# Performance work log

Hardware: AMD Instinct MI355X
Metric: run time of the kernel (lower is better)

## Reference

```python
import jax, jax.numpy as jnp
import numpy as np

NUM_EXPERTS = 32
TOP_K = 4
ALPHA = 1.702   # GPT-OSS GLU alpha
LIMIT = 7.0     # GPT-OSS clamp limit


def setup_inputs() -> dict:
    key = jax.random.key(0)
    ks = jax.random.split(key, 7)
    B, S, H, E = 2, 2048, 1024, NUM_EXPERTS
    return {
        "hidden_states": jax.random.normal(ks[0], (B, S, H), jnp.float32),
        "router_weight": jax.random.normal(ks[1], (E, H), jnp.float32) * 0.02,
        "router_bias": jax.random.normal(ks[2], (E,), jnp.float32) * 0.02,
        "gate_up_proj": jax.random.normal(ks[3], (E, H, 2 * H), jnp.float32) * 0.02,
        "gate_up_proj_bias": jax.random.normal(ks[4], (E, 2 * H), jnp.float32) * 0.02,
        "down_proj": jax.random.normal(ks[5], (E, H, H), jnp.float32) * 0.02,
        "down_proj_bias": jax.random.normal(ks[6], (E, H), jnp.float32) * 0.02,
    }


def _moe_forward(hidden_states, router_weight, router_bias,
                 gate_up_proj, gate_up_proj_bias, down_proj, down_proj_bias):
    B, S, H = hidden_states.shape
    E, K = NUM_EXPERTS, TOP_K
    T = B * S
    capacity = T * K // E * 2  # expert_capacity as in the torch module

    x = hidden_states.reshape(T, H)

    # ---- router: linear -> top-k -> softmax over top-k -> dense scatter ----
    logits = x @ router_weight.T + router_bias                     # [T, E]
    top_vals, top_idx = jax.lax.top_k(logits, K)                   # [T, K]
    weights = jax.nn.softmax(top_vals, axis=-1)                    # [T, K]
    router_scores = jnp.zeros_like(logits).at[
        jnp.arange(T)[:, None], top_idx].set(weights)              # [T, E]

    # ---- capacity-based dispatch (first-come-first-served in token order) ----
    flat_e = top_idx.reshape(-1)                                   # [T*K]
    token_id = jnp.repeat(jnp.arange(T), K)                        # [T*K]
    onehot = (flat_e[:, None] == jnp.arange(E)[None, :]).astype(jnp.int32)
    # rank of each assignment within its expert (0-based, arrival order)
    rank = jnp.take_along_axis(jnp.cumsum(onehot, axis=0),
                               flat_e[:, None], axis=1)[:, 0] - 1  # [T*K]
    valid = rank < capacity
    slot = jnp.where(valid, rank, capacity)  # out-of-range slot -> dropped

    buffer = jnp.zeros((E, capacity, H), x.dtype).at[flat_e, slot].set(
        x[token_id], mode="drop")                                  # [E, C, H]

    # ---- grouped expert MLP: gate_up GEMM + GPT-OSS GLU + down GEMM ----
    gu = jnp.einsum("ech,ehf->ecf", buffer, gate_up_proj) \
         + gate_up_proj_bias[:, None, :]                           # [E, C, 2H]
    gate = gu[..., ::2]
    up = gu[..., 1::2]
    gate = jnp.minimum(gate, LIMIT)
    up = jnp.clip(up, -LIMIT, LIMIT)
    glu = gate * jax.nn.sigmoid(gate * ALPHA)
    act = (up + 1.0) * glu                                         # [E, C, H]
    expert_out = jnp.einsum("ech,ehf->ecf", act, down_proj) \
                 + down_proj_bias[:, None, :]                      # [E, C, H]

    # ---- weighted combine (dropped tokens contribute zero) ----
    gathered = expert_out[flat_e, jnp.where(valid, rank, 0)]       # [T*K, H]
    w = router_scores[token_id, flat_e] * valid.astype(x.dtype)    # [T*K]
    out = jax.ops.segment_sum(gathered * w[:, None], token_id,
                              num_segments=T)                      # [T, H]
    return out.reshape(B, S, H), router_scores


def reference(hidden_states, router_weight, router_bias, gate_up_proj,
              gate_up_proj_bias, down_proj, down_proj_bias):
    return _moe_forward(hidden_states, router_weight, router_bias,
                        gate_up_proj, gate_up_proj_bias, down_proj,
                        down_proj_bias)
```

## Files before the change

kernel.cpp:

```cpp
#include <hip/hip_runtime.h>
#include <hip/hip_bf16.h>

#define T_TOK 4096
#define H_DIM 1024
#define E_EXP 32
#define TOPK 4
#define CAP 1024
#define PAIRS (T_TOK*TOPK)

typedef __attribute__((ext_vector_type(8))) short short8v;
typedef __attribute__((ext_vector_type(4))) float f32x4;
typedef unsigned long long u64;
typedef unsigned short ushort;

__device__ __forceinline__ float bf16_bits_to_f32(ushort h) {
    return __uint_as_float(((unsigned)h) << 16);
}
__device__ __forceinline__ unsigned bf16r(float f) {
    unsigned u = __float_as_uint(f);
    return ((u + 0x7fffu + ((u >> 16) & 1u)) >> 16) & 0xffffu;
}
__device__ __forceinline__ unsigned cvt2(float a, float b) {
    unsigned r;
    asm("v_cvt_pk_bf16_f32 %0, %1, %2" : "=v"(r) : "v"(a), "v"(b));
    return r;
}

#define GLD16(gsrc, ldst) \
    __builtin_amdgcn_global_load_lds( \
        (const __attribute__((address_space(1))) unsigned*)(gsrc), \
        (__attribute__((address_space(3))) unsigned*)(ldst), 16, 0, 0)

__global__ __launch_bounds__(256) void router_kernel(
    const float* __restrict__ x, const float* __restrict__ rw,
    const float* __restrict__ rb, float* __restrict__ scores,
    int* __restrict__ flat_e, float* __restrict__ flat_w)
{
    __shared__ float xs[H_DIM];
    __shared__ float lg[E_EXP];
    __shared__ float sw[TOPK];
    __shared__ int   se[TOPK];
    const int t = blockIdx.x;
    const int tid = threadIdx.x;

    for (int i = tid; i < H_DIM; i += 256) xs[i] = x[(size_t)t * H_DIM + i];
    __syncthreads();

    const int e = tid >> 3, l8 = tid & 7;
    float partial = 0.f;
    const float* wr = rw + (size_t)e * H_DIM;
    for (int h = l8; h < H_DIM; h += 8) partial += xs[h] * wr[h];
    partial += __shfl_xor(partial, 1);
    partial += __shfl_xor(partial, 2);
    partial += __shfl_xor(partial, 4);
    if (l8 == 0) lg[e] = partial + rb[e];
    __syncthreads();

    if (tid == 0) {
        unsigned used = 0;
        float bv[TOPK]; int bi[TOPK];
        #pragma unroll
        for (int j = 0; j < TOPK; j++) {
            float best = -1e30f; int bid = -1;
            for (int q = 0; q < E_EXP; q++) {
                if (used & (1u << q)) continue;
                if (lg[q] > best) { best = lg[q]; bid = q; }
            }
            used |= 1u << bid;
            bv[j] = best; bi[j] = bid;
        }
        const float m = bv[0];
        float s = 0.f; float w[TOPK];
        #pragma unroll
        for (int j = 0; j < TOPK; j++) { w[j] = expf(bv[j] - m); s += w[j]; }
        const float inv = 1.f / s;
        #pragma unroll
        for (int j = 0; j < TOPK; j++) { sw[j] = w[j] * inv; se[j] = bi[j]; }
    }
    __syncthreads();

    if (tid < E_EXP) {
        float v = 0.f;
        #pragma unroll
        for (int j = 0; j < TOPK; j++) if (se[j] == tid) v = sw[j];
        scores[(size_t)t * E_EXP + tid] = v;
    }
    if (tid < TOPK) {
        flat_e[t * TOPK + tid] = se[tid];
        flat_w[t * TOPK + tid] = sw[tid];
    }
}

__global__ __launch_bounds__(256) void scan_kernel(
    const int* __restrict__ flat_e, const float* __restrict__ flat_w,
    int* __restrict__ slot_token, float* __restrict__ slot_w,
    int* __restrict__ pair_slot, int* __restrict__ counts)
{
    __shared__ int cnt[256 * E_EXP];
    const int tid = threadIdx.x;
    for (int e = 0; e < E_EXP; e++) cnt[tid * E_EXP + e] = 0;
    __syncthreads();
    const int base = tid * (PAIRS / 256);
    for (int i = 0; i < PAIRS / 256; i++) {
        int e = flat_e[base + i];
        cnt[tid * E_EXP + e]++;
    }
    __syncthreads();
    if (tid < E_EXP) {
        int run = 0;
        for (int i = 0; i < 256; i++) {
            int idx = i * E_EXP + tid;
            int v = cnt[idx];
            cnt[idx] = run;
            run += v;
        }
        counts[tid] = min(run, CAP);
    }
    __syncthreads();
    for (int i = 0; i < PAIRS / 256; i++) {
        int p = base + i;
        int e = flat_e[p];
        int r = cnt[tid * E_EXP + e]++;
        if (r < CAP) {
            slot_token[e * CAP + r] = p >> 2;
            slot_w[e * CAP + r] = flat_w[p];
            pair_slot[p] = r;
        } else {
            pair_slot[p] = -1;
        }
    }
}

__global__ __launch_bounds__(256) void stage_tokens(
    const float* __restrict__ x, const int* __restrict__ slot_token,
    const int* __restrict__ counts, char* __restrict__ xbuf)
{
    const int e = blockIdx.y, rt = blockIdx.x;
    const int n = counts[e];
    const int row0 = rt * 128;
    if (row0 >= n) return;
    const int rows_here = min(128, n - row0);
    const int lane = threadIdx.x & 63, wv = threadIdx.x >> 6;
    char* tb = xbuf + ((size_t)(e * 8 + rt)) * 262144;

    for (int r = wv; r < rows_here; r += 4) {
        const float* xr = x + (size_t)slot_token[e * CAP + row0 + r] * H_DIM;
        const int s = (r >> 1) & 3;
        #pragma unroll
        for (int half = 0; half < 2; ++half) {
            int gi = half * 64 + lane;
            float4 a = *(const float4*)(xr + gi * 8);
            float4 b = *(const float4*)(xr + gi * 8 + 4);
            uint4 w;
            w.x = cvt2(a.x, a.y); w.y = cvt2(a.z, a.w);
            w.z = cvt2(b.x, b.y); w.w = cvt2(b.z, b.w);
            int t = gi >> 2, kq = gi & 3;
            *(uint4*)(tb + (size_t)t * 8192 + r * 64 + ((kq ^ s) * 16)) = w;
        }
    }
}

__global__ __launch_bounds__(256) void conv_gu(
    const float* __restrict__ wgu, char* __restrict__ wbuf)
{
    const int ct = blockIdx.x;
    const int tseg = blockIdx.y;
    const int e = blockIdx.z;
    const int lane = threadIdx.x & 63, wv = threadIdx.x >> 6;
    char* dst_base = wbuf + ((size_t)(e * 16 + ct) * 32) * 8192;
    #pragma unroll
    for (int i = 0; i < 2; ++i) {
        const int t = tseg * 8 + wv * 2 + i;
        const float* src = wgu + ((size_t)e * 1024 + t * 32) * 2048 + ct * 128 + 2 * lane;
        float2 v[32];
        #pragma unroll
        for (int k = 0; k < 32; ++k) v[k] = *(const float2*)(src + (size_t)k * 2048);
        char* dst = dst_base + (size_t)t * 8192 + lane * 16;
        #pragma unroll
        for (int kq = 0; kq < 4; ++kq) {
            uint4 g, u;
            g.x = cvt2(v[kq*8+0].x, v[kq*8+1].x); g.y = cvt2(v[kq*8+2].x, v[kq*8+3].x);
            g.z = cvt2(v[kq*8+4].x, v[kq*8+5].x); g.w = cvt2(v[kq*8+6].x, v[kq*8+7].x);
            u.x = cvt2(v[kq*8+0].y, v[kq*8+1].y); u.y = cvt2(v[kq*8+2].y, v[kq*8+3].y);
            u.z = cvt2(v[kq*8+4].y, v[kq*8+5].y); u.w = cvt2(v[kq*8+6].y, v[kq*8+7].y);
            *(uint4*)(dst + kq * 1024) = g;
            *(uint4*)(dst + 4096 + kq * 1024) = u;
        }
    }
}

__global__ __launch_bounds__(256) void conv_dn(
    const float* __restrict__ wd, char* __restrict__ wbuf)
{
    const int ct = blockIdx.x;
    const int tseg = blockIdx.y;
    const int e = blockIdx.z;
    const int lane = threadIdx.x & 63, wv = threadIdx.x >> 6;
    const int t = tseg * 4 + wv;
    const float* src = wd + ((size_t)e * 1024 + t * 32) * 1024 + ct * 128 + 2 * lane;
    float2 v[32];
    #pragma unroll
    for (int k = 0; k < 32; ++k) v[k] = *(const float2*)(src + (size_t)k * 1024);
    char* dst = wbuf + (((size_t)(e * 8 + ct) * 32) + t) * 8192 + (2 * lane) * 16;
    #pragma unroll
    for (int kq = 0; kq < 4; ++kq) {
        uint4 g0, g1;
        g0.x = cvt2(v[kq*8+0].x, v[kq*8+1].x); g0.y = cvt2(v[kq*8+2].x, v[kq*8+3].x);
        g0.z = cvt2(v[kq*8+4].x, v[kq*8+5].x); g0.w = cvt2(v[kq*8+6].x, v[kq*8+7].x);
        g1.x = cvt2(v[kq*8+0].y, v[kq*8+1].y); g1.y = cvt2(v[kq*8+2].y, v[kq*8+3].y);
        g1.z = cvt2(v[kq*8+4].y, v[kq*8+5].y); g1.w = cvt2(v[kq*8+6].y, v[kq*8+7].y);
        *(uint4*)(dst + kq * 2048) = g0;
        *(uint4*)(dst + kq * 2048 + 16) = g1;
    }
}

__global__ __launch_bounds__(256, 4) void gateup_mfma(
    const char* __restrict__ xbuf, const char* __restrict__ wbuf,
    const float* __restrict__ gub, const int* __restrict__ counts,
    char* __restrict__ act)
{
    const int lin = blockIdx.x;
    const int xcd = lin & 7, slot = lin >> 3;
    const int gg = (slot >> 3) * 8 + xcd;
    const int rt = slot & 7;
    const int e = gg >> 4, ct = gg & 15;

    const int n = counts[e];
    const int row0 = rt * 128;
    if (row0 >= n) return;
    const int rows_here = min(128, n - row0);
    const int c0f = ct * 64;

    __shared__ char AsB[2][8192];
    __shared__ char BsB[2][8192];

    const int tid = threadIdx.x;
    const int lane = tid & 63, wid = tid >> 6;
    const int wr = wid >> 1, wc = wid & 1;
    const int l15 = lane & 15, l4 = lane >> 4;

    const char* xtile = xbuf + ((size_t)(e * 8 + rt)) * 262144;
    const char* btile = wbuf + ((size_t)(e * 16 + ct) * 32) * 8192;

    f32x4 accg[4][2], accu[4][2];
    #pragma unroll
    for (int m = 0; m < 4; m++)
        #pragma unroll
        for (int j = 0; j < 2; j++) { accg[m][j] = (f32x4)0.f; accu[m][j] = (f32x4)0.f; }

    auto stage = [&](int buf, int t) {
        const char* sa = xtile + (size_t)t * 8192 + tid * 16;
        GLD16(sa, AsB[buf] + tid * 16);
        GLD16(sa + 4096, AsB[buf] + 4096 + tid * 16);
        const char* sb = btile + (size_t)t * 8192 + tid * 16;
        GLD16(sb, BsB[buf] + tid * 16);
        GLD16(sb + 4096, BsB[buf] + 4096 + tid * 16);
    };

    stage(0, 0);
    __syncthreads();
    int cur = 0;
    for (int t = 0; t < 32; ++t) {
        if (t < 31) stage(cur ^ 1, t + 1);

        short8v afr[4];
        #pragma unroll
        for (int m = 0; m < 4; ++m) {
            int row = wr * 64 + m * 16 + l15;
            afr[m] = *(short8v*)(AsB[cur] + row * 64 + ((l4 ^ ((row >> 1) & 3)) * 16));
        }
        __builtin_amdgcn_s_setprio(1);
        #pragma unroll
        for (int j = 0; j < 2; ++j) {
            int fl = wc * 32 + j * 16 + l15;
            short8v bg8 = *(short8v*)(BsB[cur] + l4 * 1024 + fl * 16);
            short8v bu8 = *(short8v*)(BsB[cur] + 4096 + l4 * 1024 + fl * 16);
            #pragma unroll
            for (int m = 0; m < 4; ++m) {
                accg[m][j] = __builtin_amdgcn_mfma_f32_16x16x32_bf16(afr[m], bg8, accg[m][j], 0, 0, 0);
                accu[m][j] = __builtin_amdgcn_mfma_f32_16x16x32_bf16(afr[m], bu8, accu[m][j], 0, 0, 0);
            }
        }
        __builtin_amdgcn_s_setprio(0);
        __syncthreads();
        cur ^= 1;
    }

    char* atile = act + ((size_t)(e * 8 + rt)) * 262144;
    #pragma unroll
    for (int j = 0; j < 2; ++j) {
        int f = c0f + wc * 32 + j * 16 + l15;
        float bgb = gub[(size_t)e * 2048 + 2 * f];
        float bub = gub[(size_t)e * 2048 + 2 * f + 1];
        int tt = f >> 5, kq = (f & 31) >> 3, ke = f & 7;
        #pragma unroll
        for (int m = 0; m < 4; ++m) {
            int rbase = wr * 64 + m * 16 + l4 * 4;
            #pragma unroll
            for (int reg = 0; reg < 4; ++reg) {
                int r = rbase + reg;
                if (r >= rows_here) continue;
                float g = accg[m][j][reg] + bgb;
                float u = accu[m][j][reg] + bub;
                g = fminf(g, 7.0f);
                u = fminf(fmaxf(u, -7.0f), 7.0f);
                float glu = g / (1.0f + __expf(-1.702f * g));
                float a = (u + 1.0f) * glu;
                *(ushort*)(atile + (size_t)tt * 8192 + r * 64 +
                           ((kq ^ ((r >> 1) & 3)) * 16) + ke * 2) = (ushort)bf16r(a);
            }
        }
    }
}

__global__ __launch_bounds__(256, 4) void down_mfma(
    const char* __restrict__ act, const char* __restrict__ wbuf,
    const float* __restrict__ db, const int* __restrict__ counts,
    ushort* __restrict__ eout)
{
    const int lin = blockIdx.x;
    const int xcd = lin & 7, slot = lin >> 3;
    const int gg = (slot >> 3) * 8 + xcd;
    const int rt = slot & 7;
    const int e = gg >> 3, ct = gg & 7;

    const int n = counts[e];
    const int row0 = rt * 128;
    if (row0 >= n) return;
    const int rows_here = min(128, n - row0);
    const int c0 = ct * 128;

    __shared__ char AsB[2][8192];
    __shared__ char BsB[2][8192];

    const int tid = threadIdx.x;
    const int lane = tid & 63, wid = tid >> 6;
    const int wr = wid >> 1, wc = wid & 1;
    const int l15 = lane & 15, l4 = lane >> 4;

    const char* atile = act + ((size_t)(e * 8 + rt)) * 262144;
    const char* btile = wbuf + ((size_t)(e * 8 + ct) * 32) * 8192;

    f32x4 acc[4][4];
    #pragma unroll
    for (int m = 0; m < 4; m++)
        #pragma unroll
        for (int j = 0; j < 4; j++) acc[m][j] = (f32x4)0.f;

    auto stage = [&](int buf, int t) {
        const char* sa = atile + (size_t)t * 8192 + tid * 16;
        GLD16(sa, AsB[buf] + tid * 16);
        GLD16(sa + 4096, AsB[buf] + 4096 + tid * 16);
        const char* sb = btile + (size_t)t * 8192 + tid * 16;
        GLD16(sb, BsB[buf] + tid * 16);
        GLD16(sb + 4096, BsB[buf] + 4096 + tid * 16);
    };

    stage(0, 0);
    __syncthreads();
    int cur = 0;
    for (int t = 0; t < 32; ++t) {
        if (t < 31) stage(cur ^ 1, t + 1);

        short8v afr[4];
        #pragma unroll
        for (int m = 0; m < 4; ++m) {
            int row = wr * 64 + m * 16 + l15;
            afr[m] = *(short8v*)(AsB[cur] + row * 64 + ((l4 ^ ((row >> 1) & 3)) * 16));
        }
        __builtin_amdgcn_s_setprio(1);
        #pragma unroll
        for (int j = 0; j < 4; ++j) {
            int nn = wc * 64 + j * 16 + l15;
            short8v b8 = *(short8v*)(BsB[cur] + l4 * 2048 + nn * 16);
            #pragma unroll
            for (int m = 0; m < 4; ++m)
                acc[m][j] = __builtin_amdgcn_mfma_f32_16x16x32_bf16(afr[m], b8, acc[m][j], 0, 0, 0);
        }
        __builtin_amdgcn_s_setprio(0);
        __syncthreads();
        cur ^= 1;
    }

    #pragma unroll
    for (int j = 0; j < 4; ++j) {
        int col = c0 + wc * 64 + j * 16 + l15;
        float bias = db[(size_t)e * H_DIM + col];
        #pragma unroll
        for (int m = 0; m < 4; ++m) {
            int rbase = wr * 64 + m * 16 + l4 * 4;
            #pragma unroll
            for (int reg = 0; reg < 4; ++reg) {
                int r = rbase + reg;
                if (r >= rows_here) continue;
                eout[((size_t)e * CAP + row0 + r) * H_DIM + col] =
                    (ushort)bf16r(acc[m][j][reg] + bias);
            }
        }
    }
}

__global__ __launch_bounds__(256) void finalize_kernel(
    const ushort* __restrict__ eout, const int* __restrict__ flat_e,
    const float* __restrict__ flat_w, const int* __restrict__ pair_slot,
    float* __restrict__ out)
{
    const int t = blockIdx.x;
    const int c = threadIdx.x * 4;
    float a0 = 0.f, a1 = 0.f, a2 = 0.f, a3 = 0.f;
    #pragma unroll
    for (int k = 0; k < TOPK; ++k) {
        int p = t * TOPK + k;
        int s = pair_slot[p];
        if (s < 0) continue;
        int e = flat_e[p];
        float w = flat_w[p];
        const ushort* row = eout + ((size_t)e * CAP + s) * H_DIM + c;
        ushort4 v = *(const ushort4*)row;
        a0 += w * bf16_bits_to_f32(v.x);
        a1 += w * bf16_bits_to_f32(v.y);
        a2 += w * bf16_bits_to_f32(v.z);
        a3 += w * bf16_bits_to_f32(v.w);
    }
    *(float4*)(out + (size_t)t * H_DIM + c) = make_float4(a0, a1, a2, a3);
}

extern "C" void kernel_launch(void* const* d_in, const int* in_sizes, int n_in,
                              void* d_out, int out_size, void* d_ws, size_t ws_size,
                              hipStream_t stream) {
    const float* x   = (const float*)d_in[0];
    const float* rw  = (const float*)d_in[1];
    const float* rb  = (const float*)d_in[2];
    const float* wgu = (const float*)d_in[3];
    const float* gub = (const float*)d_in[4];
    const float* wd  = (const float*)d_in[5];
    const float* db  = (const float*)d_in[6];

    float* out    = (float*)d_out;
    float* scores = out + (size_t)T_TOK * H_DIM;

    char* ws = (char*)d_ws;
    char* xbuf = ws;
    ushort* eout = (ushort*)ws;
    size_t off = (size_t)E_EXP * CAP * H_DIM * 2;
    char* act     = ws + off;  off += (size_t)E_EXP * CAP * H_DIM * 2;
    char* wbuf_gu = ws + off;  off += (size_t)E_EXP * 16 * 32 * 8192;
    char* wbuf_dn = ws + off;  off += (size_t)E_EXP * 8 * 32 * 8192;
    int*   flat_e     = (int*)(ws + off);   off += PAIRS * 4;
    float* flat_w     = (float*)(ws + off); off += PAIRS * 4;
    int*   slot_token = (int*)(ws + off);   off += E_EXP * CAP * 4;
    float* slot_w     = (float*)(ws + off); off += E_EXP * CAP * 4;
    int*   pair_slot  = (int*)(ws + off);   off += PAIRS * 4;
    int*   counts     = (int*)(ws + off);   off += E_EXP * 4;
    (void)ws_size; (void)out_size; (void)n_in; (void)in_sizes; (void)slot_w;

    hipLaunchKernelGGL(router_kernel, dim3(T_TOK), dim3(256), 0, stream,
                       x, rw, rb, scores, flat_e, flat_w);
    hipLaunchKernelGGL(scan_kernel, dim3(1), dim3(256), 0, stream,
                       flat_e, flat_w, slot_token, slot_w, pair_slot, counts);
    hipLaunchKernelGGL(stage_tokens, dim3(8, E_EXP), dim3(256), 0, stream,
                       x, slot_token, counts, xbuf);
    hipLaunchKernelGGL(conv_gu, dim3(16, 4, E_EXP), dim3(256), 0, stream, wgu, wbuf_gu);
    hipLaunchKernelGGL(conv_dn, dim3(8, 8, E_EXP), dim3(256), 0, stream, wd, wbuf_dn);
    hipLaunchKernelGGL(gateup_mfma, dim3(4096), dim3(256), 0, stream,
                       xbuf, wbuf_gu, gub, counts, act);
    hipLaunchKernelGGL(down_mfma, dim3(2048), dim3(256), 0, stream,
                       act, wbuf_dn, db, counts, eout);
    hipLaunchKernelGGL(finalize_kernel, dim3(T_TOK), dim3(256), 0, stream,
                       eout, flat_e, flat_w, pair_slot, out);
}
```

Baseline: 507.4 us.

## Triple-buffer LDS staging with partial vmcnt waits in MoE GEMMs

```diff
diff --git a/kernel.cpp b/kernel.cpp
--- a/kernel.cpp
+++ b/kernel.cpp
@@ -30,6 +30,11 @@
     __builtin_amdgcn_global_load_lds( \
         (const __attribute__((address_space(1))) unsigned*)(gsrc), \
         (__attribute__((address_space(3))) unsigned*)(ldst), 16, 0, 0)
+
+#define WAIT_VM4() asm volatile("s_waitcnt vmcnt(4)" ::: "memory")
+#define WAIT_VM0() asm volatile("s_waitcnt vmcnt(0)" ::: "memory")
+#define SCHEDB()   __builtin_amdgcn_sched_barrier(0)
+#define BARRIER()  __builtin_amdgcn_s_barrier()
 
 __global__ __launch_bounds__(256) void router_kernel(
     const float* __restrict__ x, const float* __restrict__ rw,
@@ -214,7 +219,7 @@
     }
 }
 
-__global__ __launch_bounds__(256, 4) void gateup_mfma(
+__global__ __launch_bounds__(256, 3) void gateup_mfma(
     const char* __restrict__ xbuf, const char* __restrict__ wbuf,
     const float* __restrict__ gub, const int* __restrict__ counts,
     char* __restrict__ act)
@@ -231,8 +236,8 @@
     const int rows_here = min(128, n - row0);
     const int c0f = ct * 64;
 
-    __shared__ char AsB[2][8192];
-    __shared__ char BsB[2][8192];
+    __shared__ char AsB[3][8192];
+    __shared__ char BsB[3][8192];
 
     const int tid = threadIdx.x;
     const int lane = tid & 63, wid = tid >> 6;
@@ -258,10 +263,13 @@
     };
 
     stage(0, 0);
-    __syncthreads();
-    int cur = 0;
+    stage(1, 1);
+    WAIT_VM4(); SCHEDB();
+    BARRIER(); SCHEDB();
+
+    int cur = 0, dst = 2;
     for (int t = 0; t < 32; ++t) {
-        if (t < 31) stage(cur ^ 1, t + 1);
+        if (t + 2 < 32) stage(dst, t + 2);
 
         short8v afr[4];
         #pragma unroll
@@ -282,8 +290,13 @@
             }
         }
         __builtin_amdgcn_s_setprio(0);
-        __syncthreads();
-        cur ^= 1;
+
+        if (t + 2 < 32) { WAIT_VM4(); }
+        else if (t + 1 < 32) { WAIT_VM0(); }
+        SCHEDB();
+        if (t + 1 < 32) { BARRIER(); SCHEDB(); }
+        cur = (cur == 2) ? 0 : cur + 1;
+        dst = (dst == 2) ? 0 : dst + 1;
     }
 
     char* atile = act + ((size_t)(e * 8 + rt)) * 262144;
@@ -313,7 +326,7 @@
     }
 }
 
-__global__ __launch_bounds__(256, 4) void down_mfma(
+__global__ __launch_bounds__(256, 3) void down_mfma(
     const char* __restrict__ act, const char* __restrict__ wbuf,
     const float* __restrict__ db, const int* __restrict__ counts,
     ushort* __restrict__ eout)
@@ -330,8 +343,8 @@
     const int rows_here = min(128, n - row0);
     const int c0 = ct * 128;
 
-    __shared__ char AsB[2][8192];
-    __shared__ char BsB[2][8192];
+    __shared__ char AsB[3][8192];
+    __shared__ char BsB[3][8192];
 
     const int tid = threadIdx.x;
     const int lane = tid & 63, wid = tid >> 6;
@@ -357,10 +370,13 @@
     };
 
     stage(0, 0);
-    __syncthreads();
-    int cur = 0;
+    stage(1, 1);
+    WAIT_VM4(); SCHEDB();
+    BARRIER(); SCHEDB();
+
+    int cur = 0, dst = 2;
     for (int t = 0; t < 32; ++t) {
-        if (t < 31) stage(cur ^ 1, t + 1);
+        if (t + 2 < 32) stage(dst, t + 2);
 
         short8v afr[4];
         #pragma unroll
@@ -378,8 +394,13 @@
                 acc[m][j] = __builtin_amdgcn_mfma_f32_16x16x32_bf16(afr[m], b8, acc[m][j], 0, 0, 0);
         }
         __builtin_amdgcn_s_setprio(0);
-        __syncthreads();
-        cur ^= 1;
+
+        if (t + 2 < 32) { WAIT_VM4(); }
+        else if (t + 1 < 32) { WAIT_VM0(); }
+        SCHEDB();
+        if (t + 1 < 32) { BARRIER(); SCHEDB(); }
+        cur = (cur == 2) ? 0 : cur + 1;
+        dst = (dst == 2) ? 0 : dst + 1;
     }
 
     #pragma unroll
```

New measurement: 530.3 us. 1.05x slower.

## Fuse gate-up weight conversion into GEMM with LDS-resident weights; batch router tokens

Applied to the files above, without the earlier changes.

```diff
diff --git a/kernel.cpp b/kernel.cpp
--- a/kernel.cpp
+++ b/kernel.cpp
@@ -31,32 +31,50 @@
         (const __attribute__((address_space(1))) unsigned*)(gsrc), \
         (__attribute__((address_space(3))) unsigned*)(ldst), 16, 0, 0)
 
+#define WAIT_VM1() asm volatile("s_waitcnt vmcnt(1)" ::: "memory")
+#define WAIT_VM0() asm volatile("s_waitcnt vmcnt(0)" ::: "memory")
+#define SCHEDB()   __builtin_amdgcn_sched_barrier(0)
+#define BARRIER()  __builtin_amdgcn_s_barrier()
+
 __global__ __launch_bounds__(256) void router_kernel(
     const float* __restrict__ x, const float* __restrict__ rw,
     const float* __restrict__ rb, float* __restrict__ scores,
     int* __restrict__ flat_e, float* __restrict__ flat_w)
 {
-    __shared__ float xs[H_DIM];
-    __shared__ float lg[E_EXP];
-    __shared__ float sw[TOPK];
-    __shared__ int   se[TOPK];
-    const int t = blockIdx.x;
+    __shared__ float xs[8][H_DIM];
+    __shared__ float lg[8][E_EXP];
+    const int t0 = blockIdx.x * 8;
     const int tid = threadIdx.x;
 
-    for (int i = tid; i < H_DIM; i += 256) xs[i] = x[(size_t)t * H_DIM + i];
+    for (int i = tid; i < 2048; i += 256) {
+        int row = i >> 8, c4 = i & 255;
+        *(float4*)&xs[row][c4 * 4] =
+            *(const float4*)(x + (size_t)(t0 + row) * H_DIM + c4 * 4);
+    }
     __syncthreads();
 
     const int e = tid >> 3, l8 = tid & 7;
-    float partial = 0.f;
-    const float* wr = rw + (size_t)e * H_DIM;
-    for (int h = l8; h < H_DIM; h += 8) partial += xs[h] * wr[h];
-    partial += __shfl_xor(partial, 1);
-    partial += __shfl_xor(partial, 2);
-    partial += __shfl_xor(partial, 4);
-    if (l8 == 0) lg[e] = partial + rb[e];
-    __syncthreads();
-
-    if (tid == 0) {
+    float part[8];
+    #pragma unroll
+    for (int tt = 0; tt < 8; ++tt) part[tt] = 0.f;
+    const float* wrow = rw + (size_t)e * H_DIM;
+    for (int h = l8; h < H_DIM; h += 8) {
+        float w = wrow[h];
+        #pragma unroll
+        for (int tt = 0; tt < 8; ++tt) part[tt] = fmaf(xs[tt][h], w, part[tt]);
+    }
+    #pragma unroll
+    for (int tt = 0; tt < 8; ++tt) {
+        float v = part[tt];
+        v += __shfl_xor(v, 1);
+        v += __shfl_xor(v, 2);
+        v += __shfl_xor(v, 4);
+        if (l8 == 0) lg[tt][e] = v + rb[e];
+    }
+    __syncthreads();
+
+    if (tid < 8) {
+        const int tt = tid, t = t0 + tt;
         unsigned used = 0;
         float bv[TOPK]; int bi[TOPK];
         #pragma unroll
@@ -64,7 +82,7 @@
             float best = -1e30f; int bid = -1;
             for (int q = 0; q < E_EXP; q++) {
                 if (used & (1u << q)) continue;
-                if (lg[q] > best) { best = lg[q]; bid = q; }
+                if (lg[tt][q] > best) { best = lg[tt][q]; bid = q; }
             }
             used |= 1u << bid;
             bv[j] = best; bi[j] = bid;
@@ -75,19 +93,18 @@
         for (int j = 0; j < TOPK; j++) { w[j] = expf(bv[j] - m); s += w[j]; }
         const float inv = 1.f / s;
         #pragma unroll
-        for (int j = 0; j < TOPK; j++) { sw[j] = w[j] * inv; se[j] = bi[j]; }
-    }
-    __syncthreads();
-
-    if (tid < E_EXP) {
-        float v = 0.f;
-        #pragma unroll
-        for (int j = 0; j < TOPK; j++) if (se[j] == tid) v = sw[j];
-        scores[(size_t)t * E_EXP + tid] = v;
-    }
-    if (tid < TOPK) {
-        flat_e[t * TOPK + tid] = se[tid];
-        flat_w[t * TOPK + tid] = sw[tid];
+        for (int j = 0; j < TOPK; j++) w[j] *= inv;
+        for (int q = 0; q < E_EXP; ++q) {
+            float v = 0.f;
+            #pragma unroll
+            for (int j = 0; j < TOPK; j++) if (bi[j] == q) v = w[j];
+            scores[(size_t)t * E_EXP + q] = v;
+        }
+        #pragma unroll
+        for (int j = 0; j < TOPK; j++) {
+            flat_e[t * TOPK + j] = bi[j];
+            flat_w[t * TOPK + j] = w[j];
+        }
     }
 }
 
@@ -160,35 +177,6 @@
     }
 }
 
-__global__ __launch_bounds__(256) void conv_gu(
-    const float* __restrict__ wgu, char* __restrict__ wbuf)
-{
-    const int ct = blockIdx.x;
-    const int tseg = blockIdx.y;
-    const int e = blockIdx.z;
-    const int lane = threadIdx.x & 63, wv = threadIdx.x >> 6;
-    char* dst_base = wbuf + ((size_t)(e * 16 + ct) * 32) * 8192;
-    #pragma unroll
-    for (int i = 0; i < 2; ++i) {
-        const int t = tseg * 8 + wv * 2 + i;
-        const float* src = wgu + ((size_t)e * 1024 + t * 32) * 2048 + ct * 128 + 2 * lane;
-        float2 v[32];
-        #pragma unroll
-        for (int k = 0; k < 32; ++k) v[k] = *(const float2*)(src + (size_t)k * 2048);
-        char* dst = dst_base + (size_t)t * 8192 + lane * 16;
-        #pragma unroll
-        for (int kq = 0; kq < 4; ++kq) {
-            uint4 g, u;
-            g.x = cvt2(v[kq*8+0].x, v[kq*8+1].x); g.y = cvt2(v[kq*8+2].x, v[kq*8+3].x);
-            g.z = cvt2(v[kq*8+4].x, v[kq*8+5].x); g.w = cvt2(v[kq*8+6].x, v[kq*8+7].x);
-            u.x = cvt2(v[kq*8+0].y, v[kq*8+1].y); u.y = cvt2(v[kq*8+2].y, v[kq*8+3].y);
-            u.z = cvt2(v[kq*8+4].y, v[kq*8+5].y); u.w = cvt2(v[kq*8+6].y, v[kq*8+7].y);
-            *(uint4*)(dst + kq * 1024) = g;
-            *(uint4*)(dst + 4096 + kq * 1024) = u;
-        }
-    }
-}
-
 __global__ __launch_bounds__(256) void conv_dn(
     const float* __restrict__ wd, char* __restrict__ wbuf)
 {
@@ -214,100 +202,116 @@
     }
 }
 
-__global__ __launch_bounds__(256, 4) void gateup_mfma(
-    const char* __restrict__ xbuf, const char* __restrict__ wbuf,
+__global__ __launch_bounds__(512, 1) void gateup_mfma(
+    const char* __restrict__ xbuf, const float* __restrict__ wgu,
     const float* __restrict__ gub, const int* __restrict__ counts,
     char* __restrict__ act)
 {
+    extern __shared__ char smem[];
+    char* Bg = smem;
+    char* Bu = smem + 65536;
+    char* As = smem + 131072;
+
     const int lin = blockIdx.x;
-    const int xcd = lin & 7, slot = lin >> 3;
-    const int gg = (slot >> 3) * 8 + xcd;
-    const int rt = slot & 7;
-    const int e = gg >> 4, ct = gg & 15;
-
+    const int e = lin >> 5, p = lin & 31;
     const int n = counts[e];
-    const int row0 = rt * 128;
-    if (row0 >= n) return;
-    const int rows_here = min(128, n - row0);
-    const int c0f = ct * 64;
-
-    __shared__ char AsB[2][8192];
-    __shared__ char BsB[2][8192];
-
+    if (n <= 0) return;
+    const int nrt = (n + 127) >> 7;
     const int tid = threadIdx.x;
+
+    {
+        const int f = tid & 31, kc = tid >> 5;
+        #pragma unroll
+        for (int g8 = 0; g8 < 8; ++g8) {
+            const int k0 = kc * 64 + g8 * 8;
+            const float* s = wgu + ((size_t)e * 1024 + k0) * 2048 + p * 64 + 2 * f;
+            float2 v[8];
+            #pragma unroll
+            for (int i = 0; i < 8; ++i) v[i] = *(const float2*)(s + (size_t)i * 2048);
+            uint4 g, u;
+            g.x = cvt2(v[0].x, v[1].x); g.y = cvt2(v[2].x, v[3].x);
+            g.z = cvt2(v[4].x, v[5].x); g.w = cvt2(v[6].x, v[7].x);
+            u.x = cvt2(v[0].y, v[1].y); u.y = cvt2(v[2].y, v[3].y);
+            u.z = cvt2(v[4].y, v[5].y); u.w = cvt2(v[6].y, v[7].y);
+            const int t = k0 >> 5, kq = (k0 >> 3) & 3;
+            const int off = t * 2048 + kq * 512 + ((f ^ (kq << 2)) * 16);
+            *(uint4*)(Bg + off) = g;
+            *(uint4*)(Bu + off) = u;
+        }
+    }
+    __syncthreads();
+
     const int lane = tid & 63, wid = tid >> 6;
     const int wr = wid >> 1, wc = wid & 1;
     const int l15 = lane & 15, l4 = lane >> 4;
-
-    const char* xtile = xbuf + ((size_t)(e * 8 + rt)) * 262144;
-    const char* btile = wbuf + ((size_t)(e * 16 + ct) * 32) * 8192;
-
-    f32x4 accg[4][2], accu[4][2];
-    #pragma unroll
-    for (int m = 0; m < 4; m++)
-        #pragma unroll
-        for (int j = 0; j < 2; j++) { accg[m][j] = (f32x4)0.f; accu[m][j] = (f32x4)0.f; }
-
-    auto stage = [&](int buf, int t) {
-        const char* sa = xtile + (size_t)t * 8192 + tid * 16;
-        GLD16(sa, AsB[buf] + tid * 16);
-        GLD16(sa + 4096, AsB[buf] + 4096 + tid * 16);
-        const char* sb = btile + (size_t)t * 8192 + tid * 16;
-        GLD16(sb, BsB[buf] + tid * 16);
-        GLD16(sb + 4096, BsB[buf] + 4096 + tid * 16);
-    };
-
-    stage(0, 0);
-    __syncthreads();
-    int cur = 0;
-    for (int t = 0; t < 32; ++t) {
-        if (t < 31) stage(cur ^ 1, t + 1);
-
-        short8v afr[4];
-        #pragma unroll
-        for (int m = 0; m < 4; ++m) {
-            int row = wr * 64 + m * 16 + l15;
-            afr[m] = *(short8v*)(AsB[cur] + row * 64 + ((l4 ^ ((row >> 1) & 3)) * 16));
-        }
-        __builtin_amdgcn_s_setprio(1);
-        #pragma unroll
-        for (int j = 0; j < 2; ++j) {
-            int fl = wc * 32 + j * 16 + l15;
-            short8v bg8 = *(short8v*)(BsB[cur] + l4 * 1024 + fl * 16);
-            short8v bu8 = *(short8v*)(BsB[cur] + 4096 + l4 * 1024 + fl * 16);
-            #pragma unroll
-            for (int m = 0; m < 4; ++m) {
-                accg[m][j] = __builtin_amdgcn_mfma_f32_16x16x32_bf16(afr[m], bg8, accg[m][j], 0, 0, 0);
-                accu[m][j] = __builtin_amdgcn_mfma_f32_16x16x32_bf16(afr[m], bu8, accu[m][j], 0, 0, 0);
+    const int fl = wc * 16 + l15;
+    const int boff = l4 * 512 + ((fl ^ (l4 << 2)) * 16);
+
+    const int fg = p * 32 + fl;
+    const float bgb = gub[(size_t)e * 2048 + 2 * fg];
+    const float bub = gub[(size_t)e * 2048 + 2 * fg + 1];
+    const int kq2 = (fg & 31) >> 3, ke = fg & 7;
+
+    for (int rt = 0; rt < nrt; ++rt) {
+        const char* xtile = xbuf + ((size_t)(e * 8 + rt)) * 262144;
+        const int rows_here = min(128, n - rt * 128);
+
+        f32x4 accg[2], accu[2];
+        accg[0] = (f32x4)0.f; accg[1] = (f32x4)0.f;
+        accu[0] = (f32x4)0.f; accu[1] = (f32x4)0.f;
+
+        __syncthreads();
+        GLD16(xtile + tid * 16, As + tid * 16);
+        GLD16(xtile + 8192 + tid * 16, As + 8192 + tid * 16);
+        WAIT_VM1(); SCHEDB();
+        BARRIER(); SCHEDB();
+
+        int cur = 0, dst = 2;
+        for (int t = 0; t < 32; ++t) {
+            if (t + 2 < 32)
+                GLD16(xtile + (size_t)(t + 2) * 8192 + tid * 16,
+                      As + dst * 8192 + tid * 16);
+
+            short8v afr[2];
+            #pragma unroll
+            for (int m = 0; m < 2; ++m) {
+                int row = wr * 32 + m * 16 + l15;
+                afr[m] = *(short8v*)(As + cur * 8192 + row * 64 +
+                                     ((l4 ^ ((row >> 1) & 3)) * 16));
             }
-        }
-        __builtin_amdgcn_s_setprio(0);
-        __syncthreads();
-        cur ^= 1;
-    }
-
-    char* atile = act + ((size_t)(e * 8 + rt)) * 262144;
-    #pragma unroll
-    for (int j = 0; j < 2; ++j) {
-        int f = c0f + wc * 32 + j * 16 + l15;
-        float bgb = gub[(size_t)e * 2048 + 2 * f];
-        float bub = gub[(size_t)e * 2048 + 2 * f + 1];
-        int tt = f >> 5, kq = (f & 31) >> 3, ke = f & 7;
-        #pragma unroll
-        for (int m = 0; m < 4; ++m) {
-            int rbase = wr * 64 + m * 16 + l4 * 4;
+            short8v bg8 = *(short8v*)(Bg + t * 2048 + boff);
+            short8v bu8 = *(short8v*)(Bu + t * 2048 + boff);
+            __builtin_amdgcn_s_setprio(1);
+            accg[0] = __builtin_amdgcn_mfma_f32_16x16x32_bf16(afr[0], bg8, accg[0], 0, 0, 0);
+            accg[1] = __builtin_amdgcn_mfma_f32_16x16x32_bf16(afr[1], bg8, accg[1], 0, 0, 0);
+            accu[0] = __builtin_amdgcn_mfma_f32_16x16x32_bf16(afr[0], bu8, accu[0], 0, 0, 0);
+            accu[1] = __builtin_amdgcn_mfma_f32_16x16x32_bf16(afr[1], bu8, accu[1], 0, 0, 0);
+            __builtin_amdgcn_s_setprio(0);
+
+            if (t + 2 < 32)      { WAIT_VM1(); }
+            else if (t + 1 < 32) { WAIT_VM0(); }
+            SCHEDB();
+            if (t + 1 < 32) { BARRIER(); SCHEDB(); }
+            cur = (cur == 2) ? 0 : cur + 1;
+            dst = (dst == 2) ? 0 : dst + 1;
+        }
+
+        char* atile = act + ((size_t)(e * 8 + rt)) * 262144;
+        #pragma unroll
+        for (int m = 0; m < 2; ++m) {
+            int rbase = wr * 32 + m * 16 + l4 * 4;
             #pragma unroll
             for (int reg = 0; reg < 4; ++reg) {
                 int r = rbase + reg;
                 if (r >= rows_here) continue;
-                float g = accg[m][j][reg] + bgb;
-                float u = accu[m][j][reg] + bub;
+                float g = accg[m][reg] + bgb;
+                float u = accu[m][reg] + bub;
                 g = fminf(g, 7.0f);
                 u = fminf(fmaxf(u, -7.0f), 7.0f);
                 float glu = g / (1.0f + __expf(-1.702f * g));
                 float a = (u + 1.0f) * glu;
-                *(ushort*)(atile + (size_t)tt * 8192 + r * 64 +
-                           ((kq ^ ((r >> 1) & 3)) * 16) + ke * 2) = (ushort)bf16r(a);
+                *(ushort*)(atile + (size_t)p * 8192 + r * 64 +
+                           ((kq2 ^ ((r >> 1) & 3)) * 16) + ke * 2) = (ushort)bf16r(a);
             }
         }
     }
@@ -444,7 +448,6 @@
     ushort* eout = (ushort*)ws;
     size_t off = (size_t)E_EXP * CAP * H_DIM * 2;
     char* act     = ws + off;  off += (size_t)E_EXP * CAP * H_DIM * 2;
-    char* wbuf_gu = ws + off;  off += (size_t)E_EXP * 16 * 32 * 8192;
     char* wbuf_dn = ws + off;  off += (size_t)E_EXP * 8 * 32 * 8192;
     int*   flat_e     = (int*)(ws + off);   off += PAIRS * 4;
     float* flat_w     = (float*)(ws + off); off += PAIRS * 4;
@@ -454,16 +457,18 @@
     int*   counts     = (int*)(ws + off);   off += E_EXP * 4;
     (void)ws_size; (void)out_size; (void)n_in; (void)in_sizes; (void)slot_w;
 
-    hipLaunchKernelGGL(router_kernel, dim3(T_TOK), dim3(256), 0, stream,
+    hipFuncSetAttribute((const void*)gateup_mfma,
+                        hipFuncAttributeMaxDynamicSharedMemorySize, 155648);
+
+    hipLaunchKernelGGL(router_kernel, dim3(T_TOK / 8), dim3(256), 0, stream,
                        x, rw, rb, scores, flat_e, flat_w);
     hipLaunchKernelGGL(scan_kernel, dim3(1), dim3(256), 0, stream,
                        flat_e, flat_w, slot_token, slot_w, pair_slot, counts);
     hipLaunchKernelGGL(stage_tokens, dim3(8, E_EXP), dim3(256), 0, stream,
                        x, slot_token, counts, xbuf);
-    hipLaunchKernelGGL(conv_gu, dim3(16, 4, E_EXP), dim3(256), 0, stream, wgu, wbuf_gu);
     hipLaunchKernelGGL(conv_dn, dim3(8, 8, E_EXP), dim3(256), 0, stream, wd, wbuf_dn);
-    hipLaunchKernelGGL(gateup_mfma, dim3(4096), dim3(256), 0, stream,
-                       xbuf, wbuf_gu, gub, counts, act);
+    hipLaunchKernelGGL(gateup_mfma, dim3(1024), dim3(512), 155648, stream,
+                       xbuf, wgu, gub, counts, act);
     hipLaunchKernelGGL(down_mfma, dim3(2048), dim3(256), 0, stream,
                        act, wbuf_dn, db, counts, eout);
     hipLaunchKernelGGL(finalize_kernel, dim3(T_TOK), dim3(256), 0, stream,
```

Result: no change. 507.5 us (+0.0%).

## Fuse weighted combine into down-proj epilogue via atomics; batch router tokens

Applied to the files above, without the earlier changes.

```diff
diff --git a/kernel.cpp b/kernel.cpp
--- a/kernel.cpp
+++ b/kernel.cpp
@@ -31,32 +31,50 @@
         (const __attribute__((address_space(1))) unsigned*)(gsrc), \
         (__attribute__((address_space(3))) unsigned*)(ldst), 16, 0, 0)
 
+__global__ void zero_kernel(float4* __restrict__ p, int n4) {
+    int i = blockIdx.x * blockDim.x + threadIdx.x;
+    if (i < n4) p[i] = make_float4(0.f, 0.f, 0.f, 0.f);
+}
+
 __global__ __launch_bounds__(256) void router_kernel(
     const float* __restrict__ x, const float* __restrict__ rw,
     const float* __restrict__ rb, float* __restrict__ scores,
     int* __restrict__ flat_e, float* __restrict__ flat_w)
 {
-    __shared__ float xs[H_DIM];
-    __shared__ float lg[E_EXP];
-    __shared__ float sw[TOPK];
-    __shared__ int   se[TOPK];
-    const int t = blockIdx.x;
+    __shared__ float xs[8][H_DIM];
+    __shared__ float lg[8][E_EXP];
+    const int t0 = blockIdx.x * 8;
     const int tid = threadIdx.x;
 
-    for (int i = tid; i < H_DIM; i += 256) xs[i] = x[(size_t)t * H_DIM + i];
+    for (int i = tid; i < 2048; i += 256) {
+        int row = i >> 8, c4 = i & 255;
+        *(float4*)&xs[row][c4 * 4] =
+            *(const float4*)(x + (size_t)(t0 + row) * H_DIM + c4 * 4);
+    }
     __syncthreads();
 
     const int e = tid >> 3, l8 = tid & 7;
-    float partial = 0.f;
-    const float* wr = rw + (size_t)e * H_DIM;
-    for (int h = l8; h < H_DIM; h += 8) partial += xs[h] * wr[h];
-    partial += __shfl_xor(partial, 1);
-    partial += __shfl_xor(partial, 2);
-    partial += __shfl_xor(partial, 4);
-    if (l8 == 0) lg[e] = partial + rb[e];
-    __syncthreads();
-
-    if (tid == 0) {
+    float part[8];
+    #pragma unroll
+    for (int tt = 0; tt < 8; ++tt) part[tt] = 0.f;
+    const float* wrow = rw + (size_t)e * H_DIM;
+    for (int h = l8; h < H_DIM; h += 8) {
+        float w = wrow[h];
+        #pragma unroll
+        for (int tt = 0; tt < 8; ++tt) part[tt] = fmaf(xs[tt][h], w, part[tt]);
+    }
+    #pragma unroll
+    for (int tt = 0; tt < 8; ++tt) {
+        float v = part[tt];
+        v += __shfl_xor(v, 1);
+        v += __shfl_xor(v, 2);
+        v += __shfl_xor(v, 4);
+        if (l8 == 0) lg[tt][e] = v + rb[e];
+    }
+    __syncthreads();
+
+    if (tid < 8) {
+        const int tt = tid, t = t0 + tt;
         unsigned used = 0;
         float bv[TOPK]; int bi[TOPK];
         #pragma unroll
@@ -64,7 +82,7 @@
             float best = -1e30f; int bid = -1;
             for (int q = 0; q < E_EXP; q++) {
                 if (used & (1u << q)) continue;
-                if (lg[q] > best) { best = lg[q]; bid = q; }
+                if (lg[tt][q] > best) { best = lg[tt][q]; bid = q; }
             }
             used |= 1u << bid;
             bv[j] = best; bi[j] = bid;
@@ -75,26 +93,25 @@
         for (int j = 0; j < TOPK; j++) { w[j] = expf(bv[j] - m); s += w[j]; }
         const float inv = 1.f / s;
         #pragma unroll
-        for (int j = 0; j < TOPK; j++) { sw[j] = w[j] * inv; se[j] = bi[j]; }
-    }
-    __syncthreads();
-
-    if (tid < E_EXP) {
-        float v = 0.f;
-        #pragma unroll
-        for (int j = 0; j < TOPK; j++) if (se[j] == tid) v = sw[j];
-        scores[(size_t)t * E_EXP + tid] = v;
-    }
-    if (tid < TOPK) {
-        flat_e[t * TOPK + tid] = se[tid];
-        flat_w[t * TOPK + tid] = sw[tid];
+        for (int j = 0; j < TOPK; j++) w[j] *= inv;
+        for (int q = 0; q < E_EXP; ++q) {
+            float v = 0.f;
+            #pragma unroll
+            for (int j = 0; j < TOPK; j++) if (bi[j] == q) v = w[j];
+            scores[(size_t)t * E_EXP + q] = v;
+        }
+        #pragma unroll
+        for (int j = 0; j < TOPK; j++) {
+            flat_e[t * TOPK + j] = bi[j];
+            flat_w[t * TOPK + j] = w[j];
+        }
     }
 }
 
 __global__ __launch_bounds__(256) void scan_kernel(
     const int* __restrict__ flat_e, const float* __restrict__ flat_w,
     int* __restrict__ slot_token, float* __restrict__ slot_w,
-    int* __restrict__ pair_slot, int* __restrict__ counts)
+    int* __restrict__ counts)
 {
     __shared__ int cnt[256 * E_EXP];
     const int tid = threadIdx.x;
@@ -124,9 +141,6 @@
         if (r < CAP) {
             slot_token[e * CAP + r] = p >> 2;
             slot_w[e * CAP + r] = flat_w[p];
-            pair_slot[p] = r;
-        } else {
-            pair_slot[p] = -1;
         }
     }
 }
@@ -316,7 +330,8 @@
 __global__ __launch_bounds__(256, 4) void down_mfma(
     const char* __restrict__ act, const char* __restrict__ wbuf,
     const float* __restrict__ db, const int* __restrict__ counts,
-    ushort* __restrict__ eout)
+    const int* __restrict__ slot_token, const float* __restrict__ slot_w,
+    float* __restrict__ out)
 {
     const int lin = blockIdx.x;
     const int xcd = lin & 7, slot = lin >> 3;
@@ -332,8 +347,17 @@
 
     __shared__ char AsB[2][8192];
     __shared__ char BsB[2][8192];
+    __shared__ int tok_s[128];
+    __shared__ float wrow_s[128];
 
     const int tid = threadIdx.x;
+    if (tid < 128) {
+        if (tid < rows_here) {
+            tok_s[tid] = slot_token[e * CAP + row0 + tid];
+            wrow_s[tid] = slot_w[e * CAP + row0 + tid];
+        } else { tok_s[tid] = 0; wrow_s[tid] = 0.f; }
+    }
+
     const int lane = tid & 63, wid = tid >> 6;
     const int wr = wid >> 1, wc = wid & 1;
     const int l15 = lane & 15, l4 = lane >> 4;
@@ -393,36 +417,11 @@
             for (int reg = 0; reg < 4; ++reg) {
                 int r = rbase + reg;
                 if (r >= rows_here) continue;
-                eout[((size_t)e * CAP + row0 + r) * H_DIM + col] =
-                    (ushort)bf16r(acc[m][j][reg] + bias);
+                atomicAdd(out + (size_t)tok_s[r] * H_DIM + col,
+                          wrow_s[r] * (acc[m][j][reg] + bias));
             }
         }
     }
-}
-
-__global__ __launch_bounds__(256) void finalize_kernel(
-    const ushort* __restrict__ eout, const int* __restrict__ flat_e,
-    const float* __restrict__ flat_w, const int* __restrict__ pair_slot,
-    float* __restrict__ out)
-{
-    const int t = blockIdx.x;
-    const int c = threadIdx.x * 4;
-    float a0 = 0.f, a1 = 0.f, a2 = 0.f, a3 = 0.f;
-    #pragma unroll
-    for (int k = 0; k < TOPK; ++k) {
-        int p = t * TOPK + k;
-        int s = pair_slot[p];
-        if (s < 0) continue;
-        int e = flat_e[p];
-        float w = flat_w[p];
-        const ushort* row = eout + ((size_t)e * CAP + s) * H_DIM + c;
-        ushort4 v = *(const ushort4*)row;
-        a0 += w * bf16_bits_to_f32(v.x);
-        a1 += w * bf16_bits_to_f32(v.y);
-        a2 += w * bf16_bits_to_f32(v.z);
-        a3 += w * bf16_bits_to_f32(v.w);
-    }
-    *(float4*)(out + (size_t)t * H_DIM + c) = make_float4(a0, a1, a2, a3);
 }
 
 extern "C" void kernel_launch(void* const* d_in, const int* in_sizes, int n_in,
@@ -441,7 +440,6 @@
 
     char* ws = (char*)d_ws;
     char* xbuf = ws;
-    ushort* eout = (ushort*)ws;
     size_t off = (size_t)E_EXP * CAP * H_DIM * 2;
     char* act     = ws + off;  off += (size_t)E_EXP * CAP * H_DIM * 2;
     char* wbuf_gu = ws + off;  off += (size_t)E_EXP * 16 * 32 * 8192;
@@ -450,14 +448,15 @@
     float* flat_w     = (float*)(ws + off); off += PAIRS * 4;
     int*   slot_token = (int*)(ws + off);   off += E_EXP * CAP * 4;
     float* slot_w     = (float*)(ws + off); off += E_EXP * CAP * 4;
-    int*   pair_slot  = (int*)(ws + off);   off += PAIRS * 4;
     int*   counts     = (int*)(ws + off);   off += E_EXP * 4;
-    (void)ws_size; (void)out_size; (void)n_in; (void)in_sizes; (void)slot_w;
-
-    hipLaunchKernelGGL(router_kernel, dim3(T_TOK), dim3(256), 0, stream,
+    (void)ws_size; (void)out_size; (void)n_in; (void)in_sizes;
+
+    hipLaunchKernelGGL(zero_kernel, dim3(4096), dim3(256), 0, stream,
+                       (float4*)out, (T_TOK * H_DIM) / 4);
+    hipLaunchKernelGGL(router_kernel, dim3(T_TOK / 8), dim3(256), 0, stream,
                        x, rw, rb, scores, flat_e, flat_w);
     hipLaunchKernelGGL(scan_kernel, dim3(1), dim3(256), 0, stream,
-                       flat_e, flat_w, slot_token, slot_w, pair_slot, counts);
+                       flat_e, flat_w, slot_token, slot_w, counts);
     hipLaunchKernelGGL(stage_tokens, dim3(8, E_EXP), dim3(256), 0, stream,
                        x, slot_token, counts, xbuf);
     hipLaunchKernelGGL(conv_gu, dim3(16, 4, E_EXP), dim3(256), 0, stream, wgu, wbuf_gu);
@@ -465,7 +464,5 @@
     hipLaunchKernelGGL(gateup_mfma, dim3(4096), dim3(256), 0, stream,
                        xbuf, wbuf_gu, gub, counts, act);
     hipLaunchKernelGGL(down_mfma, dim3(2048), dim3(256), 0, stream,
-                       act, wbuf_dn, db, counts, eout);
-    hipLaunchKernelGGL(finalize_kernel, dim3(T_TOK), dim3(256), 0, stream,
-                       eout, flat_e, flat_w, pair_slot, out);
-}
+                       act, wbuf_dn, db, counts, slot_token, slot_w, out);
+}
```

Measured after the change: 506.8 us. About the same (-0.1%).
